# Optimization experiments

Hardware: AMD Instinct MI355X
Metric: run time of the kernel (lower is better)

## Reference

```python
import jax, jax.numpy as jnp
import numpy as np

X_SIZE = 256
H_SIZE = 512
N_CHILDREN = 32768


def setup_inputs() -> dict:
    key = jax.random.key(0)
    ks = jax.random.split(key, 7)
    x = jax.random.normal(ks[0], (X_SIZE,), dtype=jnp.float32)
    hs = jax.random.normal(ks[1], (N_CHILDREN, H_SIZE), dtype=jnp.float32)
    cs = jax.random.normal(ks[2], (N_CHILDREN, H_SIZE), dtype=jnp.float32)
    # xavier-uniform-ish init for weights, zeros for biases
    def xavier(k, shape):
        fan_in, fan_out = shape[-1], shape[-2]
        limit = float(np.sqrt(6.0 / (fan_in + fan_out)))
        return jax.random.uniform(k, shape, jnp.float32, -limit, limit)
    w_iou = xavier(ks[3], (3, H_SIZE, X_SIZE))
    u_iou = xavier(ks[4], (3, H_SIZE, H_SIZE))
    b_iou = jnp.zeros((3, H_SIZE), jnp.float32)
    w_f = xavier(ks[5], (H_SIZE, X_SIZE))
    u_f = xavier(ks[6], (H_SIZE, H_SIZE))
    b_f = jnp.zeros((H_SIZE, 1), jnp.float32)
    return {"x": x, "hs": hs, "cs": cs, "w_iou": w_iou, "u_iou": u_iou,
            "b_iou": b_iou, "w_f": w_f, "u_f": u_f, "b_f": b_f}


def reference(x, hs, cs, w_iou, u_iou, b_iou, w_f, u_f, b_f):
    # Child-sum Tree-LSTM cell for a single node.
    h_sum = hs.sum(axis=0)                                    # (h,)
    iou = (jnp.einsum('khx,x->kh', w_iou, x)
           + jnp.einsum('khg,g->kh', u_iou, h_sum)
           + b_iou)                                            # (3, h)
    i, o, u = iou[0], iou[1], iou[2]
    # fs: (h, n_children) forget gates, one per child
    fs = (w_f @ x)[:, None] + jnp.einsum('hg,ng->hn', u_f, hs) + b_f
    i = jax.nn.sigmoid(i)
    o = jax.nn.sigmoid(o)
    fs = jax.nn.sigmoid(fs)
    u = jnp.tanh(u)
    c = i * u + jnp.sum(fs * cs.T, axis=1)                    # (h,)
    h = o * jnp.tanh(c)
    return (h, c)
```

## Files before the change

### kernel.cpp

```cpp
#include <hip/hip_runtime.h>
#include <stdint.h>
#include <stddef.h>

#define H 512
#define XD 256
#define NCHLD 32768
#define NB 64
#define NCT 4
#define NRT 4
#define LDSP 520
#define NSHARD 4

#define WS_PREF 0
#define WS_CACC 512
#define WS_HSUM 2560
#define WS_IOU  4608
#define WS_UF16 8192

typedef float f32x4 __attribute__((ext_vector_type(4)));
typedef _Float16 f16x8 __attribute__((ext_vector_type(8)));
typedef _Float16 f16x4 __attribute__((ext_vector_type(4)));

__device__ __forceinline__ float sigm(float x) { return 1.0f / (1.0f + __expf(-x)); }

__global__ __launch_bounds__(256) void k0_setup(const float* __restrict__ x,
                                                const float* __restrict__ w_f,
                                                const float* __restrict__ b_f,
                                                const float* __restrict__ u_f,
                                                float* __restrict__ ws) {
    const int b = blockIdx.x;
    if (b < 256) {
        const int i = (b * 256 + threadIdx.x) * 4;
        float4 v = *(const float4*)(u_f + i);
        f16x4 h;
        h[0] = (_Float16)v.x; h[1] = (_Float16)v.y;
        h[2] = (_Float16)v.z; h[3] = (_Float16)v.w;
        *(f16x4*)((_Float16*)(ws + WS_UF16) + i) = h;
    } else {
        const int gid = (b - 256) * 256 + threadIdx.x;
        const int row = gid >> 2;
        const int part = gid & 3;
        const float4* wr = (const float4*)(w_f + (size_t)row * XD) + part * 16;
        const float4* xv = (const float4*)x + part * 16;
        float acc = 0.0f;
#pragma unroll 4
        for (int i = 0; i < 16; ++i) {
            float4 a = wr[i], c = xv[i];
            acc += a.x * c.x + a.y * c.y + a.z * c.z + a.w * c.w;
        }
        acc += __shfl_xor(acc, 1);
        acc += __shfl_xor(acc, 2);
        if (part == 0) ws[WS_PREF + row] = acc + b_f[row];
        if (gid < 512) {
            ((float4*)(ws + WS_CACC))[gid] = make_float4(0.f, 0.f, 0.f, 0.f);
            ((float4*)(ws + WS_HSUM))[gid] = make_float4(0.f, 0.f, 0.f, 0.f);
        }
    }
}

__global__ __launch_bounds__(512, 4) void k2_main(const float* __restrict__ hs,
                                                  const float* __restrict__ cs,
                                                  float* __restrict__ ws) {
    __shared__ _Float16 bt[NB][LDSP];
    __shared__ float hsum_l[H];

    const _Float16* uf16 = (const _Float16*)(ws + WS_UF16);
    const float* pre_f = ws + WS_PREF;
    float* c_acc = ws + WS_CACC + (blockIdx.x & (NSHARD - 1)) * H;
    float* h_sum = ws + WS_HSUM + (blockIdx.x & (NSHARD - 1)) * H;

    const int tid  = threadIdx.x;
    const int wid  = tid >> 6;
    const int lane = tid & 63;
    const int c0   = blockIdx.x * NB;

    const int sc = tid >> 3;
    const int sg = tid & 7;
    const float* hsrc = hs + (size_t)(c0 + sc) * H + sg * 4;
    _Float16* stp = &bt[sc][sg * 4];

    if (tid < H) hsum_l[tid] = 0.0f;
    __syncthreads();

    float4 r[8];
#pragma unroll
    for (int s = 0; s < 8; ++s) r[s] = *(const float4*)(hsrc + (size_t)s * 32);

#define STAGE_SLICE(vv, s)                                                        \
    {                                                                             \
        f16x4 hq;                                                                 \
        hq[0] = (_Float16)(vv).x; hq[1] = (_Float16)(vv).y;                       \
        hq[2] = (_Float16)(vv).z; hq[3] = (_Float16)(vv).w;                       \
        *(f16x4*)(stp + (s) * 32) = hq;                                           \
        float4 v = (vv);                                                          \
        v.x += __shfl_xor(v.x, 8);  v.y += __shfl_xor(v.y, 8);                    \
        v.z += __shfl_xor(v.z, 8);  v.w += __shfl_xor(v.w, 8);                    \
        v.x += __shfl_xor(v.x, 16); v.y += __shfl_xor(v.y, 16);                   \
        v.z += __shfl_xor(v.z, 16); v.w += __shfl_xor(v.w, 16);                   \
        v.x += __shfl_xor(v.x, 32); v.y += __shfl_xor(v.y, 32);                   \
        v.z += __shfl_xor(v.z, 32); v.w += __shfl_xor(v.w, 32);                   \
        if (lane < 8) {                                                           \
            const int d = (s) * 32 + sg * 4;                                      \
            atomicAdd(&hsum_l[d + 0], v.x); atomicAdd(&hsum_l[d + 1], v.y);       \
            atomicAdd(&hsum_l[d + 2], v.z); atomicAdd(&hsum_l[d + 3], v.w);       \
        }                                                                         \
    }

#pragma unroll
    for (int s = 0; s < 8; ++s) {
        float4 vv = r[s];
        r[s] = *(const float4*)(hsrc + (size_t)(s + 8) * 32);
        STAGE_SLICE(vv, s)
    }
#pragma unroll
    for (int s = 0; s < 8; ++s) {
        STAGE_SLICE(r[s], s + 8)
    }
#undef STAGE_SLICE

    __syncthreads();

    atomicAdd(&h_sum[tid], hsum_l[tid]);

    f32x4 acc[NRT][NCT];
    const f32x4 vzero = {0.0f, 0.0f, 0.0f, 0.0f};
#pragma unroll
    for (int rt = 0; rt < NRT; ++rt)
#pragma unroll
        for (int ct = 0; ct < NCT; ++ct)
            acc[rt][ct] = vzero;

    const int arow = wid * 64 + (lane & 15);
    const int ak   = (lane >> 4) * 8;
    const _Float16* abase = uf16 + (size_t)arow * H + ak;
    const int bcol = lane & 15;
    const int bk   = (lane >> 4) * 8;

#pragma unroll
    for (int kk = 0; kk < 16; ++kk) {
        f16x8 af[NRT];
#pragma unroll
        for (int rt = 0; rt < NRT; ++rt)
            af[rt] = *(const f16x8*)(abase + (size_t)rt * 16 * H + kk * 32);
#pragma unroll
        for (int ct = 0; ct < NCT; ++ct) {
            f16x8 bf = *(const f16x8*)(&bt[ct * 16 + bcol][kk * 32 + bk]);
#pragma unroll
            for (int rt = 0; rt < NRT; ++rt)
                acc[rt][ct] = __builtin_amdgcn_mfma_f32_16x16x32_f16(af[rt], bf, acc[rt][ct], 0, 0, 0);
        }
    }

    const int g4 = (lane >> 4) * 4;
#pragma unroll
    for (int rt = 0; rt < NRT; ++rt) {
        const int rbase = wid * 64 + rt * 16 + g4;
        float4 pf = *(const float4*)(pre_f + rbase);
        f32x4 csum = vzero;
#pragma unroll
        for (int ct = 0; ct < NCT; ++ct) {
            const int child = c0 + ct * 16 + (lane & 15);
            float4 cv = *(const float4*)(cs + (size_t)child * H + rbase);
            csum[0] += sigm(acc[rt][ct][0] + pf.x) * cv.x;
            csum[1] += sigm(acc[rt][ct][1] + pf.y) * cv.y;
            csum[2] += sigm(acc[rt][ct][2] + pf.z) * cv.z;
            csum[3] += sigm(acc[rt][ct][3] + pf.w) * cv.w;
        }
#pragma unroll
        for (int m = 1; m <= 8; m <<= 1) {
            csum[0] += __shfl_xor(csum[0], m); csum[1] += __shfl_xor(csum[1], m);
            csum[2] += __shfl_xor(csum[2], m); csum[3] += __shfl_xor(csum[3], m);
        }
        if ((lane & 15) == 0) {
            atomicAdd(&c_acc[rbase + 0], csum[0]); atomicAdd(&c_acc[rbase + 1], csum[1]);
            atomicAdd(&c_acc[rbase + 2], csum[2]); atomicAdd(&c_acc[rbase + 3], csum[3]);
        }
    }
}

__global__ __launch_bounds__(256) void k3_iou(const float* __restrict__ x,
                                              const float* __restrict__ w_iou,
                                              const float* __restrict__ u_iou,
                                              const float* __restrict__ b_iou,
                                              float* __restrict__ ws) {
    const int gid = blockIdx.x * 256 + threadIdx.x;
    const int row = gid >> 4;
    const int part = gid & 15;
    float acc = 0.0f;
    const float4* wr = (const float4*)(w_iou + (size_t)row * XD) + part * 4;
    const float4* xv = (const float4*)x + part * 4;
#pragma unroll
    for (int i = 0; i < 4; ++i) {
        float4 a = wr[i], b = xv[i];
        acc += a.x * b.x + a.y * b.y + a.z * b.z + a.w * b.w;
    }
    const float4* ur = (const float4*)(u_iou + (size_t)row * H) + part * 8;
    const float4* h0 = (const float4*)(ws + WS_HSUM) + part * 8;
    const float4* h1 = h0 + 128;
    const float4* h2 = h1 + 128;
    const float4* h3 = h2 + 128;
#pragma unroll
    for (int i = 0; i < 8; ++i) {
        float4 a = ur[i];
        float4 b0 = h0[i], b1 = h1[i], b2 = h2[i], b3 = h3[i];
        acc += a.x * (b0.x + b1.x + b2.x + b3.x);
        acc += a.y * (b0.y + b1.y + b2.y + b3.y);
        acc += a.z * (b0.z + b1.z + b2.z + b3.z);
        acc += a.w * (b0.w + b1.w + b2.w + b3.w);
    }
    acc += __shfl_xor(acc, 1);
    acc += __shfl_xor(acc, 2);
    acc += __shfl_xor(acc, 4);
    acc += __shfl_xor(acc, 8);
    if (part == 0) ws[WS_IOU + row] = acc + b_iou[row];
}

__global__ __launch_bounds__(512) void k4_fin(const float* __restrict__ ws,
                                              float* __restrict__ out) {
    const int h = threadIdx.x;
    const float i = sigm(ws[WS_IOU + h]);
    const float o = sigm(ws[WS_IOU + 512 + h]);
    const float u = tanhf(ws[WS_IOU + 1024 + h]);
    const float cacc = ws[WS_CACC + h] + ws[WS_CACC + 512 + h] +
                       ws[WS_CACC + 1024 + h] + ws[WS_CACC + 1536 + h];
    const float c = i * u + cacc;
    out[h]       = o * tanhf(c);
    out[512 + h] = c;
}

extern "C" void kernel_launch(void* const* d_in, const int* in_sizes, int n_in,
                              void* d_out, int out_size, void* d_ws, size_t ws_size,
                              hipStream_t stream) {
    const float* x     = (const float*)d_in[0];
    const float* hs    = (const float*)d_in[1];
    const float* cs    = (const float*)d_in[2];
    const float* w_iou = (const float*)d_in[3];
    const float* u_iou = (const float*)d_in[4];
    const float* b_iou = (const float*)d_in[5];
    const float* w_f   = (const float*)d_in[6];
    const float* u_f   = (const float*)d_in[7];
    const float* b_f   = (const float*)d_in[8];
    float* ws  = (float*)d_ws;
    float* out = (float*)d_out;

    k0_setup<<<264, 256, 0, stream>>>(x, w_f, b_f, u_f, ws);
    k2_main<<<NCHLD / NB, 512, 0, stream>>>(hs, cs, ws);
    k3_iou<<<96, 256, 0, stream>>>(x, w_iou, u_iou, b_iou, ws);
    k4_fin<<<1, 512, 0, stream>>>(ws, out);
}
```

Measured before the change: 209.3 us.

## Retile forget-gate GEMM into 128x128 blocks with double-buffered LDS staging of U_f

The main kernel changes from 64-child blocks that each stream all of fp16 U_f from global memory to 128x128 output tiles. It walks K in 8 phases with double-buffered LDS: U_f goes in through global_load_lds with an XOR swizzle, and hs is converted to fp16 in registers one phase ahead. This cuts the per-block U_f traffic and overlaps loads with MFMA work. In exchange, each hs row is now read by four row-tile blocks, and only one of them builds the h_sum. Accumulation shards grow from 4 to 32 to reduce atomic contention, and k3/k4 now reduce all 32 shards.

```diff
diff --git a/kernel.cpp b/kernel.cpp
--- a/kernel.cpp
+++ b/kernel.cpp
@@ -5,23 +5,30 @@
 #define H 512
 #define XD 256
 #define NCHLD 32768
-#define NB 64
-#define NCT 4
-#define NRT 4
-#define LDSP 520
-#define NSHARD 4
+#define BM 128
+#define BN 128
+#define KTP 64
+#define NPH 8
+#define BP 68
+#define NSHARD 32
 
 #define WS_PREF 0
-#define WS_CACC 512
-#define WS_HSUM 2560
-#define WS_IOU  4608
-#define WS_UF16 8192
+#define WS_IOU  512
+#define WS_CACC 2048
+#define WS_HSUM 18432
+#define WS_UF16 34816
 
 typedef float f32x4 __attribute__((ext_vector_type(4)));
 typedef _Float16 f16x8 __attribute__((ext_vector_type(8)));
 typedef _Float16 f16x4 __attribute__((ext_vector_type(4)));
 
 __device__ __forceinline__ float sigm(float x) { return 1.0f / (1.0f + __expf(-x)); }
+
+__device__ __forceinline__ void gload_lds16(const _Float16* g, void* l) {
+    __builtin_amdgcn_global_load_lds((const __attribute__((address_space(1))) void*)g,
+                                     (__attribute__((address_space(3))) void*)l,
+                                     16, 0, 0);
+}
 
 __global__ __launch_bounds__(256) void k0_setup(const float* __restrict__ x,
                                                 const float* __restrict__ w_f,
@@ -51,116 +58,161 @@
         acc += __shfl_xor(acc, 1);
         acc += __shfl_xor(acc, 2);
         if (part == 0) ws[WS_PREF + row] = acc + b_f[row];
-        if (gid < 512) {
-            ((float4*)(ws + WS_CACC))[gid] = make_float4(0.f, 0.f, 0.f, 0.f);
-            ((float4*)(ws + WS_HSUM))[gid] = make_float4(0.f, 0.f, 0.f, 0.f);
-        }
+        float4 z = make_float4(0.f, 0.f, 0.f, 0.f);
+#pragma unroll
+        for (int t = 0; t < 4; ++t)
+            ((float4*)ws)[512 + gid * 4 + t] = z;
     }
 }
 
 __global__ __launch_bounds__(512, 4) void k2_main(const float* __restrict__ hs,
                                                   const float* __restrict__ cs,
                                                   float* __restrict__ ws) {
-    __shared__ _Float16 bt[NB][LDSP];
+    __shared__ _Float16 As[2][BM * 64];
+    __shared__ _Float16 Bs[2][BN][BP];
     __shared__ float hsum_l[H];
 
     const _Float16* uf16 = (const _Float16*)(ws + WS_UF16);
     const float* pre_f = ws + WS_PREF;
-    float* c_acc = ws + WS_CACC + (blockIdx.x & (NSHARD - 1)) * H;
-    float* h_sum = ws + WS_HSUM + (blockIdx.x & (NSHARD - 1)) * H;
+    const int bid   = blockIdx.x;
+    const int ntile = bid >> 2;
+    const int mtile = bid & 3;
+    const int c0    = ntile * BN;
+    const int r0    = mtile * BM;
 
     const int tid  = threadIdx.x;
     const int wid  = tid >> 6;
     const int lane = tid & 63;
-    const int c0   = blockIdx.x * NB;
-
-    const int sc = tid >> 3;
-    const int sg = tid & 7;
-    const float* hsrc = hs + (size_t)(c0 + sc) * H + sg * 4;
-    _Float16* stp = &bt[sc][sg * 4];
-
+
+    const int ch = tid >> 2;
+    const int kq = tid & 3;
+    const float4* bsrc = (const float4*)(hs + (size_t)(c0 + ch) * H) + kq * 4;
+
+    const int dd0  = wid * 128 + lane;
+    const int row0 = dd0 >> 3;
+    const int sl0  = (dd0 & 7) ^ (row0 & 7);
+    const _Float16* asrc0 = uf16 + (size_t)(r0 + row0) * H + sl0 * 8;
+    const int dd1  = dd0 + 64;
+    const int row1 = dd1 >> 3;
+    const int sl1  = (dd1 & 7) ^ (row1 & 7);
+    const _Float16* asrc1 = uf16 + (size_t)(r0 + row1) * H + sl1 * 8;
+
+    const int wm = wid >> 1;
+    const int wn = wid & 1;
+    const int fc = lane & 15;
+    const int q  = lane >> 4;
+
+#define ISSUE_A(p, buf)                                                          \
+    {                                                                            \
+        gload_lds16(asrc0 + (p) * KTP, (char*)&As[buf][0] + (wid * 128) * 16);   \
+        gload_lds16(asrc1 + (p) * KTP, (char*)&As[buf][0] + (wid * 128 + 64) * 16); \
+    }
+
+#define WRITE_B(p, buf, b0, b1, b2, b3)                                          \
+    {                                                                            \
+        _Float16* bd = &Bs[buf][ch][kq * 16];                                    \
+        f16x8 lo, hi;                                                            \
+        lo[0] = (_Float16)(b0).x; lo[1] = (_Float16)(b0).y;                      \
+        lo[2] = (_Float16)(b0).z; lo[3] = (_Float16)(b0).w;                      \
+        lo[4] = (_Float16)(b1).x; lo[5] = (_Float16)(b1).y;                      \
+        lo[6] = (_Float16)(b1).z; lo[7] = (_Float16)(b1).w;                      \
+        hi[0] = (_Float16)(b2).x; hi[1] = (_Float16)(b2).y;                      \
+        hi[2] = (_Float16)(b2).z; hi[3] = (_Float16)(b2).w;                      \
+        hi[4] = (_Float16)(b3).x; hi[5] = (_Float16)(b3).y;                      \
+        hi[6] = (_Float16)(b3).z; hi[7] = (_Float16)(b3).w;                      \
+        *(f16x8*)bd = lo;                                                        \
+        *(f16x8*)(bd + 8) = hi;                                                  \
+        if (mtile == 0) {                                                        \
+            float4 v0 = b0, v1 = b1, v2 = b2, v3 = b3;                           \
+            _Pragma("unroll")                                                    \
+            for (int m = 4; m <= 32; m <<= 1) {                                  \
+                v0.x += __shfl_xor(v0.x, m); v0.y += __shfl_xor(v0.y, m);        \
+                v0.z += __shfl_xor(v0.z, m); v0.w += __shfl_xor(v0.w, m);        \
+                v1.x += __shfl_xor(v1.x, m); v1.y += __shfl_xor(v1.y, m);        \
+                v1.z += __shfl_xor(v1.z, m); v1.w += __shfl_xor(v1.w, m);        \
+                v2.x += __shfl_xor(v2.x, m); v2.y += __shfl_xor(v2.y, m);        \
+                v2.z += __shfl_xor(v2.z, m); v2.w += __shfl_xor(v2.w, m);        \
+                v3.x += __shfl_xor(v3.x, m); v3.y += __shfl_xor(v3.y, m);        \
+                v3.z += __shfl_xor(v3.z, m); v3.w += __shfl_xor(v3.w, m);        \
+            }                                                                    \
+            if (lane < 4) {                                                      \
+                float* hd = &hsum_l[(p) * KTP + lane * 16];                      \
+                atomicAdd(hd + 0,  v0.x); atomicAdd(hd + 1,  v0.y);              \
+                atomicAdd(hd + 2,  v0.z); atomicAdd(hd + 3,  v0.w);              \
+                atomicAdd(hd + 4,  v1.x); atomicAdd(hd + 5,  v1.y);              \
+                atomicAdd(hd + 6,  v1.z); atomicAdd(hd + 7,  v1.w);              \
+                atomicAdd(hd + 8,  v2.x); atomicAdd(hd + 9,  v2.y);              \
+                atomicAdd(hd + 10, v2.z); atomicAdd(hd + 11, v2.w);              \
+                atomicAdd(hd + 12, v3.x); atomicAdd(hd + 13, v3.y);              \
+                atomicAdd(hd + 14, v3.z); atomicAdd(hd + 15, v3.w);              \
+            }                                                                    \
+        }                                                                        \
+    }
+
+    ISSUE_A(0, 0)
+    float4 b0 = bsrc[0], b1 = bsrc[1], b2 = bsrc[2], b3 = bsrc[3];
     if (tid < H) hsum_l[tid] = 0.0f;
     __syncthreads();
-
-    float4 r[8];
-#pragma unroll
-    for (int s = 0; s < 8; ++s) r[s] = *(const float4*)(hsrc + (size_t)s * 32);
-
-#define STAGE_SLICE(vv, s)                                                        \
-    {                                                                             \
-        f16x4 hq;                                                                 \
-        hq[0] = (_Float16)(vv).x; hq[1] = (_Float16)(vv).y;                       \
-        hq[2] = (_Float16)(vv).z; hq[3] = (_Float16)(vv).w;                       \
-        *(f16x4*)(stp + (s) * 32) = hq;                                           \
-        float4 v = (vv);                                                          \
-        v.x += __shfl_xor(v.x, 8);  v.y += __shfl_xor(v.y, 8);                    \
-        v.z += __shfl_xor(v.z, 8);  v.w += __shfl_xor(v.w, 8);                    \
-        v.x += __shfl_xor(v.x, 16); v.y += __shfl_xor(v.y, 16);                   \
-        v.z += __shfl_xor(v.z, 16); v.w += __shfl_xor(v.w, 16);                   \
-        v.x += __shfl_xor(v.x, 32); v.y += __shfl_xor(v.y, 32);                   \
-        v.z += __shfl_xor(v.z, 32); v.w += __shfl_xor(v.w, 32);                   \
-        if (lane < 8) {                                                           \
-            const int d = (s) * 32 + sg * 4;                                      \
-            atomicAdd(&hsum_l[d + 0], v.x); atomicAdd(&hsum_l[d + 1], v.y);       \
-            atomicAdd(&hsum_l[d + 2], v.z); atomicAdd(&hsum_l[d + 3], v.w);       \
-        }                                                                         \
-    }
-
-#pragma unroll
-    for (int s = 0; s < 8; ++s) {
-        float4 vv = r[s];
-        r[s] = *(const float4*)(hsrc + (size_t)(s + 8) * 32);
-        STAGE_SLICE(vv, s)
-    }
-#pragma unroll
-    for (int s = 0; s < 8; ++s) {
-        STAGE_SLICE(r[s], s + 8)
-    }
-#undef STAGE_SLICE
-
+    WRITE_B(0, 0, b0, b1, b2, b3)
     __syncthreads();
 
-    atomicAdd(&h_sum[tid], hsum_l[tid]);
-
-    f32x4 acc[NRT][NCT];
+    f32x4 acc[2][4];
     const f32x4 vzero = {0.0f, 0.0f, 0.0f, 0.0f};
 #pragma unroll
-    for (int rt = 0; rt < NRT; ++rt)
-#pragma unroll
-        for (int ct = 0; ct < NCT; ++ct)
+    for (int rt = 0; rt < 2; ++rt)
+#pragma unroll
+        for (int ct = 0; ct < 4; ++ct)
             acc[rt][ct] = vzero;
 
-    const int arow = wid * 64 + (lane & 15);
-    const int ak   = (lane >> 4) * 8;
-    const _Float16* abase = uf16 + (size_t)arow * H + ak;
-    const int bcol = lane & 15;
-    const int bk   = (lane >> 4) * 8;
-
-#pragma unroll
-    for (int kk = 0; kk < 16; ++kk) {
-        f16x8 af[NRT];
-#pragma unroll
-        for (int rt = 0; rt < NRT; ++rt)
-            af[rt] = *(const f16x8*)(abase + (size_t)rt * 16 * H + kk * 32);
-#pragma unroll
-        for (int ct = 0; ct < NCT; ++ct) {
-            f16x8 bf = *(const f16x8*)(&bt[ct * 16 + bcol][kk * 32 + bk]);
-#pragma unroll
-            for (int rt = 0; rt < NRT; ++rt)
-                acc[rt][ct] = __builtin_amdgcn_mfma_f32_16x16x32_f16(af[rt], bf, acc[rt][ct], 0, 0, 0);
-        }
-    }
-
-    const int g4 = (lane >> 4) * 4;
-#pragma unroll
-    for (int rt = 0; rt < NRT; ++rt) {
-        const int rbase = wid * 64 + rt * 16 + g4;
-        float4 pf = *(const float4*)(pre_f + rbase);
+    int cur = 0;
+#pragma unroll
+    for (int p = 0; p < NPH; ++p) {
+        float4 n0, n1, n2, n3;
+        if (p + 1 < NPH) {
+            ISSUE_A(p + 1, cur ^ 1)
+            const float4* bs = bsrc + (p + 1) * 16;
+            n0 = bs[0]; n1 = bs[1]; n2 = bs[2]; n3 = bs[3];
+        }
+
+#pragma unroll
+        for (int kk = 0; kk < 2; ++kk) {
+            f16x8 af[2];
+#pragma unroll
+            for (int rt = 0; rt < 2; ++rt) {
+                const int ar  = wm * 32 + rt * 16 + fc;
+                const int seg = (kk * 4 + q) ^ (ar & 7);
+                af[rt] = *(const f16x8*)((const char*)&As[cur][0] + ar * 128 + seg * 16);
+            }
+#pragma unroll
+            for (int ct = 0; ct < 4; ++ct) {
+                const f16x8 bf = *(const f16x8*)(&Bs[cur][wn * 64 + ct * 16 + fc][kk * 32 + q * 8]);
+                acc[0][ct] = __builtin_amdgcn_mfma_f32_16x16x32_f16(af[0], bf, acc[0][ct], 0, 0, 0);
+                acc[1][ct] = __builtin_amdgcn_mfma_f32_16x16x32_f16(af[1], bf, acc[1][ct], 0, 0, 0);
+            }
+        }
+
+        if (p + 1 < NPH) {
+            WRITE_B(p + 1, cur ^ 1, n0, n1, n2, n3)
+            __syncthreads();
+            cur ^= 1;
+        }
+    }
+#undef ISSUE_A
+#undef WRITE_B
+
+    if (mtile == 0)
+        atomicAdd(&ws[WS_HSUM + (ntile & (NSHARD - 1)) * H + tid], hsum_l[tid]);
+
+    float* c_acc = ws + WS_CACC + (bid & (NSHARD - 1)) * H;
+#pragma unroll
+    for (int rt = 0; rt < 2; ++rt) {
+        const int rglob = r0 + wm * 32 + rt * 16 + q * 4;
+        float4 pf = *(const float4*)(pre_f + rglob);
         f32x4 csum = vzero;
 #pragma unroll
-        for (int ct = 0; ct < NCT; ++ct) {
-            const int child = c0 + ct * 16 + (lane & 15);
-            float4 cv = *(const float4*)(cs + (size_t)child * H + rbase);
+        for (int ct = 0; ct < 4; ++ct) {
+            const int child = c0 + wn * 64 + ct * 16 + fc;
+            float4 cv = *(const float4*)(cs + (size_t)child * H + rglob);
             csum[0] += sigm(acc[rt][ct][0] + pf.x) * cv.x;
             csum[1] += sigm(acc[rt][ct][1] + pf.y) * cv.y;
             csum[2] += sigm(acc[rt][ct][2] + pf.z) * cv.z;
@@ -171,9 +223,9 @@
             csum[0] += __shfl_xor(csum[0], m); csum[1] += __shfl_xor(csum[1], m);
             csum[2] += __shfl_xor(csum[2], m); csum[3] += __shfl_xor(csum[3], m);
         }
-        if ((lane & 15) == 0) {
-            atomicAdd(&c_acc[rbase + 0], csum[0]); atomicAdd(&c_acc[rbase + 1], csum[1]);
-            atomicAdd(&c_acc[rbase + 2], csum[2]); atomicAdd(&c_acc[rbase + 3], csum[3]);
+        if (fc == 0) {
+            atomicAdd(&c_acc[rglob + 0], csum[0]); atomicAdd(&c_acc[rglob + 1], csum[1]);
+            atomicAdd(&c_acc[rglob + 2], csum[2]); atomicAdd(&c_acc[rglob + 3], csum[3]);
         }
     }
 }
@@ -183,7 +235,21 @@
                                               const float* __restrict__ u_iou,
                                               const float* __restrict__ b_iou,
                                               float* __restrict__ ws) {
-    const int gid = blockIdx.x * 256 + threadIdx.x;
+    __shared__ float h_red[H];
+    const int tid = threadIdx.x;
+    {
+        float a0 = 0.0f, a1 = 0.0f;
+#pragma unroll 8
+        for (int s = 0; s < NSHARD; ++s) {
+            a0 += ws[WS_HSUM + s * H + tid * 2 + 0];
+            a1 += ws[WS_HSUM + s * H + tid * 2 + 1];
+        }
+        h_red[tid * 2 + 0] = a0;
+        h_red[tid * 2 + 1] = a1;
+    }
+    __syncthreads();
+
+    const int gid = blockIdx.x * 256 + tid;
     const int row = gid >> 4;
     const int part = gid & 15;
     float acc = 0.0f;
@@ -195,18 +261,11 @@
         acc += a.x * b.x + a.y * b.y + a.z * b.z + a.w * b.w;
     }
     const float4* ur = (const float4*)(u_iou + (size_t)row * H) + part * 8;
-    const float4* h0 = (const float4*)(ws + WS_HSUM) + part * 8;
-    const float4* h1 = h0 + 128;
-    const float4* h2 = h1 + 128;
-    const float4* h3 = h2 + 128;
+    const float4* hv = (const float4*)h_red + part * 8;
 #pragma unroll
     for (int i = 0; i < 8; ++i) {
-        float4 a = ur[i];
-        float4 b0 = h0[i], b1 = h1[i], b2 = h2[i], b3 = h3[i];
-        acc += a.x * (b0.x + b1.x + b2.x + b3.x);
-        acc += a.y * (b0.y + b1.y + b2.y + b3.y);
-        acc += a.z * (b0.z + b1.z + b2.z + b3.z);
-        acc += a.w * (b0.w + b1.w + b2.w + b3.w);
+        float4 a = ur[i], b = hv[i];
+        acc += a.x * b.x + a.y * b.y + a.z * b.z + a.w * b.w;
     }
     acc += __shfl_xor(acc, 1);
     acc += __shfl_xor(acc, 2);
@@ -218,11 +277,12 @@
 __global__ __launch_bounds__(512) void k4_fin(const float* __restrict__ ws,
                                               float* __restrict__ out) {
     const int h = threadIdx.x;
+    float cacc = 0.0f;
+#pragma unroll 8
+    for (int s = 0; s < NSHARD; ++s) cacc += ws[WS_CACC + s * H + h];
     const float i = sigm(ws[WS_IOU + h]);
     const float o = sigm(ws[WS_IOU + 512 + h]);
     const float u = tanhf(ws[WS_IOU + 1024 + h]);
-    const float cacc = ws[WS_CACC + h] + ws[WS_CACC + 512 + h] +
-                       ws[WS_CACC + 1024 + h] + ws[WS_CACC + 1536 + h];
     const float c = i * u + cacc;
     out[h]       = o * tanhf(c);
     out[512 + h] = c;
@@ -244,7 +304,7 @@
     float* out = (float*)d_out;
 
     k0_setup<<<264, 256, 0, stream>>>(x, w_f, b_f, u_f, ws);
-    k2_main<<<NCHLD / NB, 512, 0, stream>>>(hs, cs, ws);
+    k2_main<<<(NCHLD / BN) * (H / BM), 512, 0, stream>>>(hs, cs, ws);
     k3_iou<<<96, 256, 0, stream>>>(x, w_iou, u_iou, b_iou, ws);
     k4_fin<<<1, 512, 0, stream>>>(ws, out);
 }
```

New measurement: 251.8 us. +20.3%, slower.
